# Optimization experiments

Hardware: AMD Instinct MI355X
Metric: run time of the kernel (lower is better)

## Reference

```python
import jax, jax.numpy as jnp
import numpy as np

HEADS = 16
D_K = 64  # hidden_units // heads


def setup_inputs() -> dict:
    key = jax.random.key(0)
    ks = jax.random.split(key, 9)
    B, S, D, H = 4, 2048, 1024, 1024  # batch, seq, in_shape, hidden_units
    inputs = jax.random.normal(ks[0], (B, S, D), dtype=jnp.float32)
    # xavier_normal for weights, default bias init ~ small uniform (use zeros for simplicity of baseline? keep uniform like torch)
    def xavier(k, fan_in, fan_out):
        std = jnp.sqrt(2.0 / (fan_in + fan_out))
        return jax.random.normal(k, (fan_out, fan_in), dtype=jnp.float32) * std
    Wq = xavier(ks[1], D, H)
    Wk = xavier(ks[2], D, H)
    Wv = xavier(ks[3], D, H)
    Wo = xavier(ks[4], H, H)
    bound = 1.0 / jnp.sqrt(D)
    bq = jax.random.uniform(ks[5], (H,), minval=-bound, maxval=bound, dtype=jnp.float32)
    bk = jax.random.uniform(ks[6], (H,), minval=-bound, maxval=bound, dtype=jnp.float32)
    bv = jax.random.uniform(ks[7], (H,), minval=-bound, maxval=bound, dtype=jnp.float32)
    bo = jax.random.uniform(ks[8], (H,), minval=-1.0 / jnp.sqrt(H), maxval=1.0 / jnp.sqrt(H), dtype=jnp.float32)
    return {"inputs": inputs, "Wq": Wq, "bq": bq, "Wk": Wk, "bk": bk,
            "Wv": Wv, "bv": bv, "Wo": Wo, "bo": bo}


def reference(inputs, Wq, bq, Wk, bk, Wv, bv, Wo, bo):
    B, S, _ = inputs.shape
    # QKV projections -> (B, S, heads, d_k)
    def proj(W, b):
        return (inputs @ W.T + b).reshape(B, S, HEADS, D_K)
    q = proj(Wq, bq)
    k = proj(Wk, bk)
    v = proj(Wv, bv)
    scale = 1.0 / jnp.sqrt(jnp.float32(D_K))
    # scores: (B, heads, S, S)
    scores = jnp.einsum('bqhd,bkhd->bhqk', q, k) * scale
    attn = jax.nn.softmax(scores, axis=-1)
    # (B, heads, S, d_k) -> (B, S, heads*d_k)
    ctx = jnp.einsum('bhqk,bkhd->bqhd', attn, v).reshape(B, S, HEADS * D_K)
    out = ctx @ Wo.T + bo
    return out
```

## Files before the change

kernel.cpp:

```cpp
#include <hip/hip_runtime.h>
#include <stdint.h>


using bf16x8 = __attribute__((ext_vector_type(8))) short;
using f32x4  = __attribute__((ext_vector_type(4))) float;

#define QSCALE 0.18033688f

__device__ __forceinline__ unsigned short f2bf(float f) {
    unsigned u = __builtin_bit_cast(unsigned, f);
    u += 0x7fffu + ((u >> 16) & 1u);
    return (unsigned short)(u >> 16);
}

__device__ __forceinline__ unsigned pack2bf(float f0, float f1) {
    unsigned u0 = __builtin_bit_cast(unsigned, f0) + 0x8000u;
    unsigned u1 = __builtin_bit_cast(unsigned, f1) + 0x8000u;
    return __builtin_amdgcn_perm(u1, u0, 0x07060302);
}

__device__ __forceinline__ void gld16(const void* g, void* l) {
    void* gnc = (void*)g;
    __builtin_amdgcn_global_load_lds((__attribute__((address_space(1))) void*)gnc,
                                     (__attribute__((address_space(3))) void*)l,
                                     16, 0, 0);
}

__device__ __forceinline__ int swz(int R, int g) {
    return R * 64 + ((g ^ (R & 7)) << 3);
}

__global__ void castall(const float* __restrict__ X, const float* __restrict__ Wq,
                        const float* __restrict__ Wk, const float* __restrict__ Wv,
                        const float* __restrict__ Wo, unsigned short* __restrict__ Xb,
                        unsigned short* __restrict__ Wqkvb, unsigned short* __restrict__ Wob) {
    const int bx = blockIdx.x;
    const float* src; unsigned short* dst; int idx;
    if (bx < 8192) { src = X; dst = Xb; idx = bx * 256 + threadIdx.x; }
    else {
        const int r = bx - 8192, w = r >> 10;
        idx = (r & 1023) * 256 + threadIdx.x;
        src = (w == 0) ? Wq : (w == 1) ? Wk : (w == 2) ? Wv : Wo;
        dst = (w == 3) ? Wob : Wqkvb + (size_t)w * 1048576;
    }
    float4 v = ((const float4*)src)[idx];
    ((uint2*)dst)[idx] = make_uint2(pack2bf(v.x, v.y), pack2bf(v.z, v.w));
}

__global__ __launch_bounds__(256) void gemm_qkv(const unsigned short* __restrict__ A,
                                                const unsigned short* __restrict__ Wqkv,
                                                const float* __restrict__ bq,
                                                const float* __restrict__ bk,
                                                const float* __restrict__ bv,
                                                unsigned short* __restrict__ Qb,
                                                unsigned short* __restrict__ Kb,
                                                unsigned short* __restrict__ Vt) {
    __shared__ alignas(16) unsigned short smem[17408];
    unsigned short* sA = smem;
    unsigned short* sB = smem + 8192;
    unsigned short* OT = smem;

    const int tid  = threadIdx.x;
    const int lane = tid & 63;
    const int wave = tid >> 6;
    const int quad = lane >> 4;
    const int l15  = lane & 15;
    const int lr   = lane >> 3;
    const int lcs  = (((lane & 7) ^ lr) << 3);
    const int nb   = blockIdx.x >> 3;
    const int col0 = (blockIdx.x & 7) * 128;
    const int row0 = blockIdx.y * 128;
    const unsigned short* W = Wqkv + ((size_t)nb << 20);
    const float* bias = (nb == 0) ? bq : (nb == 1) ? bk : bv;
    const int wm = wave >> 1, wn = wave & 1;

    f32x4 acc[4][4];
#pragma unroll
    for (int i = 0; i < 4; i++)
#pragma unroll
        for (int j = 0; j < 4; j++) acc[i][j] = f32x4{0.f, 0.f, 0.f, 0.f};

    for (int kt = 0; kt < 16; ++kt) {
        const int k0 = kt * 64;
#pragma unroll
        for (int i = 0; i < 4; i++) {
            const int c = wave * 4 + i;
            const int r = c * 8 + lr;
            gld16(A + (size_t)(row0 + r) * 1024 + k0 + lcs, &sA[c * 512]);
            gld16(W + (size_t)(col0 + r) * 1024 + k0 + lcs, &sB[c * 512]);
        }
        __syncthreads();
#pragma unroll
        for (int kx = 0; kx < 2; ++kx) {
            bf16x8 a[4], b[4];
#pragma unroll
            for (int i = 0; i < 4; i++) {
                a[i] = *(const bf16x8*)&sA[swz(wm * 64 + i * 16 + l15, kx * 4 + quad)];
                b[i] = *(const bf16x8*)&sB[swz(wn * 64 + i * 16 + l15, kx * 4 + quad)];
            }
#pragma unroll
            for (int i = 0; i < 4; i++)
#pragma unroll
                for (int j = 0; j < 4; j++)
                    acc[i][j] = __builtin_amdgcn_mfma_f32_16x16x32_bf16(a[i], b[j], acc[i][j], 0, 0, 0);
        }
        __syncthreads();
    }

    if (nb != 2) {
        const float sc = (nb == 0) ? QSCALE : 1.0f;
#pragma unroll
        for (int i = 0; i < 4; i++) {
#pragma unroll
            for (int j = 0; j < 4; j++) {
                const int ct  = wn * 64 + j * 16 + l15;
                const float bvv = bias[col0 + ct];
                const int rt  = wm * 64 + i * 16 + quad * 4;
#pragma unroll
                for (int r = 0; r < 4; r++)
                    OT[(rt + r) * 136 + ct] = f2bf((acc[i][j][r] + bvv) * sc);
            }
        }
    } else {
#pragma unroll
        for (int i = 0; i < 4; i++) {
#pragma unroll
            for (int j = 0; j < 4; j++) {
                const int ct  = wn * 64 + j * 16 + l15;
                const float bvv = bias[col0 + ct];
                const int rt  = wm * 64 + i * 16 + quad * 4;
                *(uint2*)&OT[ct * 136 + rt] =
                    make_uint2(pack2bf(acc[i][j][0] + bvv, acc[i][j][1] + bvv),
                               pack2bf(acc[i][j][2] + bvv, acc[i][j][3] + bvv));
            }
        }
    }
    __syncthreads();

    const int rr   = wave * 32 + (lane >> 1);
    const int half = lane & 1;
    if (nb != 2) {
        unsigned short* C = (nb == 0) ? Qb : Kb;
        unsigned short* gdst = C + (size_t)(row0 + rr) * 1024 + col0 + half * 64;
#pragma unroll
        for (int k = 0; k < 8; k++)
            *(bf16x8*)(gdst + k * 8) = *(const bf16x8*)&OT[rr * 136 + half * 64 + k * 8];
    } else {
        const int bb = row0 >> 11, s0l = row0 & 2047;
        unsigned short* gdst = Vt + ((size_t)(bb * 1024 + col0 + rr)) * 2048 + s0l + half * 64;
#pragma unroll
        for (int k = 0; k < 8; k++)
            *(bf16x8*)(gdst + k * 8) = *(const bf16x8*)&OT[rr * 136 + half * 64 + k * 8];
    }
}

__global__ __launch_bounds__(256) void gemm_out(const unsigned short* __restrict__ A,
                                                const unsigned short* __restrict__ W,
                                                const float* __restrict__ bias,
                                                float* __restrict__ C) {
    __shared__ alignas(16) unsigned short sA[128 * 64];
    __shared__ alignas(16) unsigned short sB[128 * 64];
    const int tid  = threadIdx.x;
    const int lane = tid & 63;
    const int wave = tid >> 6;
    const int quad = lane >> 4;
    const int l15  = lane & 15;
    const int lr   = lane >> 3;
    const int lcs  = (((lane & 7) ^ lr) << 3);
    const int row0 = blockIdx.y * 128;
    const int col0 = blockIdx.x * 128;
    const int wm = wave >> 1, wn = wave & 1;

    f32x4 acc[4][4];
#pragma unroll
    for (int i = 0; i < 4; i++)
#pragma unroll
        for (int j = 0; j < 4; j++) acc[i][j] = f32x4{0.f, 0.f, 0.f, 0.f};

    for (int kt = 0; kt < 16; ++kt) {
        const int k0 = kt * 64;
#pragma unroll
        for (int i = 0; i < 4; i++) {
            const int c = wave * 4 + i;
            const int r = c * 8 + lr;
            gld16(A + (size_t)(row0 + r) * 1024 + k0 + lcs, &sA[c * 512]);
            gld16(W + (size_t)(col0 + r) * 1024 + k0 + lcs, &sB[c * 512]);
        }
        __syncthreads();
#pragma unroll
        for (int kx = 0; kx < 2; ++kx) {
            bf16x8 a[4], b[4];
#pragma unroll
            for (int i = 0; i < 4; i++) {
                a[i] = *(const bf16x8*)&sA[swz(wm * 64 + i * 16 + l15, kx * 4 + quad)];
                b[i] = *(const bf16x8*)&sB[swz(wn * 64 + i * 16 + l15, kx * 4 + quad)];
            }
#pragma unroll
            for (int i = 0; i < 4; i++)
#pragma unroll
                for (int j = 0; j < 4; j++)
                    acc[i][j] = __builtin_amdgcn_mfma_f32_16x16x32_bf16(a[i], b[j], acc[i][j], 0, 0, 0);
        }
        __syncthreads();
    }

#pragma unroll
    for (int i = 0; i < 4; i++) {
#pragma unroll
        for (int j = 0; j < 4; j++) {
            const int col   = col0 + wn * 64 + j * 16 + l15;
            const float bvv = bias[col];
            const int rbase = row0 + wm * 64 + i * 16 + quad * 4;
#pragma unroll
            for (int r = 0; r < 4; r++)
                C[(size_t)(rbase + r) * 1024 + col] = acc[i][j][r] + bvv;
        }
    }
}

__global__ __launch_bounds__(512) void attn(const unsigned short* __restrict__ Q,
                                            const unsigned short* __restrict__ K,
                                            const unsigned short* __restrict__ Vt,
                                            unsigned short* __restrict__ Ctx) {
    __shared__ alignas(16) unsigned short Kl[2][4096];
    __shared__ alignas(16) unsigned short Vl[2][4096];
    __shared__ alignas(16) unsigned short Pl[8][32][72];

    const int tid  = threadIdx.x;
    const int lane = tid & 63;
    const int wave = tid >> 6;
    const int quad = lane >> 4;
    const int l15  = lane & 15;
    const int lr   = lane >> 3;
    const int lcs  = (((lane & 7) ^ lr) << 3);

    const int qt = blockIdx.x, h = blockIdx.y, b = blockIdx.z;
    const int q0 = qt * 256;
    const size_t tokbase = (size_t)b * 2048;

    bf16x8 qa[2][2];
#pragma unroll
    for (int mt = 0; mt < 2; ++mt)
#pragma unroll
        for (int kx = 0; kx < 2; ++kx)
            qa[mt][kx] = *(const bf16x8*)(Q + (tokbase + q0 + wave * 32 + mt * 16 + l15) * 1024 +
                                          h * 64 + kx * 32 + quad * 8);

    f32x4 O[2][4], Osum[2];
#pragma unroll
    for (int mt = 0; mt < 2; ++mt) {
#pragma unroll
        for (int nt = 0; nt < 4; ++nt) O[mt][nt] = f32x4{0.f, 0.f, 0.f, 0.f};
        Osum[mt] = f32x4{0.f, 0.f, 0.f, 0.f};
    }
    const bf16x8 vones = {16256, 16256, 16256, 16256, 16256, 16256, 16256, 16256};

#define AT_STAGE(kt_, buf_)                                                                     \
    {                                                                                           \
        const int rr = wave * 8 + lr;                                                           \
        gld16(K + (tokbase + (kt_) * 64 + rr) * 1024 + h * 64 + lcs, &Kl[buf_][wave * 512]);    \
        gld16(Vt + ((size_t)(b * 1024 + h * 64 + rr)) * 2048 + (kt_) * 64 + lcs,                \
              &Vl[buf_][wave * 512]);                                                           \
    }

    AT_STAGE(0, 0)
    for (int kt = 0; kt < 32; ++kt) {
        const int buf = kt & 1;
        __syncthreads();
        if (kt < 31) AT_STAGE(kt + 1, buf ^ 1)

        f32x4 St[4][2];
#pragma unroll
        for (int nt = 0; nt < 4; ++nt)
#pragma unroll
            for (int mt = 0; mt < 2; ++mt) St[nt][mt] = f32x4{0.f, 0.f, 0.f, 0.f};
#pragma unroll
        for (int kx = 0; kx < 2; ++kx) {
            bf16x8 kb[4];
#pragma unroll
            for (int nt = 0; nt < 4; ++nt)
                kb[nt] = *(const bf16x8*)&Kl[buf][swz(nt * 16 + l15, kx * 4 + quad)];
#pragma unroll
            for (int nt = 0; nt < 4; ++nt)
#pragma unroll
                for (int mt = 0; mt < 2; ++mt)
                    St[nt][mt] = __builtin_amdgcn_mfma_f32_16x16x32_bf16(kb[nt], qa[mt][kx], St[nt][mt], 0, 0, 0);
        }

#pragma unroll
        for (int mt = 0; mt < 2; ++mt) {
#pragma unroll
            for (int nt = 0; nt < 4; ++nt) {
                float p0 = __builtin_amdgcn_exp2f(St[nt][mt][0]);
                float p1 = __builtin_amdgcn_exp2f(St[nt][mt][1]);
                float p2 = __builtin_amdgcn_exp2f(St[nt][mt][2]);
                float p3 = __builtin_amdgcn_exp2f(St[nt][mt][3]);
                *(uint2*)&Pl[wave][mt * 16 + l15][nt * 16 + quad * 4] =
                    make_uint2(pack2bf(p0, p1), pack2bf(p2, p3));
            }
        }

#pragma unroll
        for (int kx = 0; kx < 2; ++kx) {
            bf16x8 pa[2], vb[4];
#pragma unroll
            for (int mt = 0; mt < 2; ++mt)
                pa[mt] = *(const bf16x8*)&Pl[wave][mt * 16 + l15][kx * 32 + quad * 8];
#pragma unroll
            for (int nt = 0; nt < 4; ++nt)
                vb[nt] = *(const bf16x8*)&Vl[buf][swz(nt * 16 + l15, kx * 4 + quad)];
#pragma unroll
            for (int mt = 0; mt < 2; ++mt) {
#pragma unroll
                for (int nt = 0; nt < 4; ++nt)
                    O[mt][nt] = __builtin_amdgcn_mfma_f32_16x16x32_bf16(pa[mt], vb[nt], O[mt][nt], 0, 0, 0);
                Osum[mt] = __builtin_amdgcn_mfma_f32_16x16x32_bf16(pa[mt], vones, Osum[mt], 0, 0, 0);
            }
        }
    }
#undef AT_STAGE

#pragma unroll
    for (int mt = 0; mt < 2; ++mt) {
#pragma unroll
        for (int r = 0; r < 4; ++r) {
            const float inv = 1.0f / Osum[mt][r];
            const int row   = q0 + wave * 32 + mt * 16 + quad * 4 + r;
            const size_t base = (tokbase + row) * 1024 + h * 64;
#pragma unroll
            for (int nt = 0; nt < 4; ++nt)
                Ctx[base + nt * 16 + l15] = f2bf(O[mt][nt][r] * inv);
        }
    }
}

extern "C" void kernel_launch(void* const* d_in, const int* in_sizes, int n_in,
                              void* d_out, int out_size, void* d_ws, size_t ws_size,
                              hipStream_t stream) {
    (void)in_sizes; (void)n_in; (void)out_size; (void)ws_size;
    const float* X  = (const float*)d_in[0];
    const float* Wq = (const float*)d_in[1];
    const float* bq = (const float*)d_in[2];
    const float* Wk = (const float*)d_in[3];
    const float* bk = (const float*)d_in[4];
    const float* Wv = (const float*)d_in[5];
    const float* bv = (const float*)d_in[6];
    const float* Wo = (const float*)d_in[7];
    const float* bo = (const float*)d_in[8];

    char* ws = (char*)d_ws;
    unsigned short* Xb    = (unsigned short*)(ws);
    unsigned short* Qb    = (unsigned short*)(ws + (size_t)16 * 1048576);
    unsigned short* Kb    = (unsigned short*)(ws + (size_t)32 * 1048576);
    unsigned short* Vt    = (unsigned short*)(ws + (size_t)48 * 1048576);
    unsigned short* Wqkvb = (unsigned short*)(ws + (size_t)64 * 1048576);
    unsigned short* Wob   = (unsigned short*)(ws + (size_t)70 * 1048576);
    unsigned short* Ctx   = Xb;

    castall<<<dim3(12288), 256, 0, stream>>>(X, Wq, Wk, Wv, Wo, Xb, Wqkvb, Wob);
    gemm_qkv<<<dim3(24, 64), 256, 0, stream>>>(Xb, Wqkvb, bq, bk, bv, Qb, Kb, Vt);
    attn<<<dim3(8, 16, 4), 512, 0, stream>>>(Qb, Kb, Vt, Ctx);
    gemm_out<<<dim3(8, 64), 256, 0, stream>>>(Ctx, Wob, bo, (float*)d_out);
}
```

Baseline: 277.1 us.

## Rewrite QKV GEMM with 256x256 tiles and double-buffered async LDS pipeline

The QKV projection GEMM moves from 128x128 tiles with 4 waves and a synchronous load-then-compute loop to 256x256 tiles with 8 waves, using 128KB of LDS as two buffers. Global-to-LDS loads for the next k-tile are interleaved with MFMA phases, paced by explicit vmcnt waits and barriers, and MFMA bursts run at raised wave priority. This targets memory latency stalls and raises data reuse per tile. The trade-off is fewer blocks (384), more registers and LDS per block, and an epilogue split into two halves.

Measured after the change: 293.1 us. 5.8% more time.

```diff
diff --git a/kernel.cpp b/kernel.cpp
--- a/kernel.cpp
+++ b/kernel.cpp
@@ -47,110 +47,159 @@
     ((uint2*)dst)[idx] = make_uint2(pack2bf(v.x, v.y), pack2bf(v.z, v.w));
 }
 
-__global__ __launch_bounds__(256) void gemm_qkv(const unsigned short* __restrict__ A,
-                                                const unsigned short* __restrict__ Wqkv,
-                                                const float* __restrict__ bq,
-                                                const float* __restrict__ bk,
-                                                const float* __restrict__ bv,
-                                                unsigned short* __restrict__ Qb,
-                                                unsigned short* __restrict__ Kb,
-                                                unsigned short* __restrict__ Vt) {
-    __shared__ alignas(16) unsigned short smem[17408];
-    unsigned short* sA = smem;
-    unsigned short* sB = smem + 8192;
-    unsigned short* OT = smem;
+__global__ __launch_bounds__(512, 2) void gemm_qkv(const unsigned short* __restrict__ A,
+                                                   const unsigned short* __restrict__ Wqkv,
+                                                   const float* __restrict__ bq,
+                                                   const float* __restrict__ bk,
+                                                   const float* __restrict__ bv,
+                                                   unsigned short* __restrict__ Qb,
+                                                   unsigned short* __restrict__ Kb,
+                                                   unsigned short* __restrict__ Vt) {
+    __shared__ alignas(16) unsigned short smem[65536];
 
     const int tid  = threadIdx.x;
     const int lane = tid & 63;
-    const int wave = tid >> 6;
+    const int w    = tid >> 6;
     const int quad = lane >> 4;
     const int l15  = lane & 15;
     const int lr   = lane >> 3;
     const int lcs  = (((lane & 7) ^ lr) << 3);
-    const int nb   = blockIdx.x >> 3;
-    const int col0 = (blockIdx.x & 7) * 128;
-    const int row0 = blockIdx.y * 128;
-    const unsigned short* W = Wqkv + ((size_t)nb << 20);
+    const int wm   = w >> 2;
+    const int wn   = w & 3;
+
+    const int col0 = blockIdx.x * 256;
+    const int row0 = blockIdx.y * 256;
+
+    const unsigned short* aS = A    + (size_t)(row0 + w * 16 + lr) * 1024 + lcs;
+    const unsigned short* bS = Wqkv + (size_t)(col0 + w * 16 + lr) * 1024 + lcs;
+    const int dstW = w * 1024;
+
+#define STG_A(t_, h_, b_)                                                              \
+    { const unsigned short* s_ = aS + (size_t)(h_) * 131072 + (t_) * 64;               \
+      gld16(s_,            &smem[(b_) * 32768 + (h_) * 8192 + dstW]);                  \
+      gld16(s_ + 8 * 1024, &smem[(b_) * 32768 + (h_) * 8192 + dstW + 512]); }
+#define STG_B(t_, h_, b_)                                                              \
+    { const unsigned short* s_ = bS + (size_t)(h_) * 131072 + (t_) * 64;               \
+      gld16(s_,            &smem[(b_) * 32768 + 16384 + (h_) * 8192 + dstW]);          \
+      gld16(s_ + 8 * 1024, &smem[(b_) * 32768 + 16384 + (h_) * 8192 + dstW + 512]); }
+
+    f32x4 acc[8][4];
+#pragma unroll
+    for (int i = 0; i < 8; i++)
+#pragma unroll
+        for (int j = 0; j < 4; j++) acc[i][j] = f32x4{0.f, 0.f, 0.f, 0.f};
+
+    STG_A(0, 0, 0) STG_A(0, 1, 0) STG_B(0, 0, 0) STG_B(0, 1, 0)
+    STG_B(1, 0, 1) STG_B(1, 1, 1)
+    asm volatile("s_waitcnt vmcnt(4)" ::: "memory");
+    __builtin_amdgcn_s_barrier();
+
+    for (int t = 0; t < 16; ++t) {
+        const int b = t & 1;
+        unsigned short* bufA = smem + b * 32768;
+        unsigned short* bufB = bufA + 16384;
+        bf16x8 bfr[4][2];
+#pragma unroll
+        for (int p = 0; p < 4; ++p) {
+            bf16x8 afr[2][2];
+            if (p == 0) {
+#pragma unroll
+                for (int nf = 0; nf < 4; ++nf)
+#pragma unroll
+                    for (int kx = 0; kx < 2; ++kx)
+                        bfr[nf][kx] = *(const bf16x8*)&bufB[swz(wn * 64 + nf * 16 + l15, kx * 4 + quad)];
+            }
+#pragma unroll
+            for (int mi = 0; mi < 2; ++mi)
+#pragma unroll
+                for (int kx = 0; kx < 2; ++kx)
+                    afr[mi][kx] = *(const bf16x8*)&bufA[swz(wm * 128 + (p * 2 + mi) * 16 + l15, kx * 4 + quad)];
+
+            if (p == 0)      { if (t < 15) STG_A(t + 1, 0, b ^ 1) }
+            else if (p == 1) { if (t < 15) STG_A(t + 1, 1, b ^ 1) }
+            else if (p == 2) { if (t < 14) STG_B(t + 2, 0, b) }
+            else {
+                if (t < 14) {
+                    STG_B(t + 2, 1, b)
+                    asm volatile("s_waitcnt vmcnt(4)" ::: "memory");
+                } else if (t == 14) {
+                    asm volatile("s_waitcnt vmcnt(0)" ::: "memory");
+                }
+            }
+            __builtin_amdgcn_s_barrier();
+            asm volatile("s_waitcnt lgkmcnt(0)" ::: "memory");
+            __builtin_amdgcn_sched_barrier(0);
+            __builtin_amdgcn_s_setprio(1);
+#pragma unroll
+            for (int kx = 0; kx < 2; ++kx)
+#pragma unroll
+                for (int mi = 0; mi < 2; ++mi)
+#pragma unroll
+                    for (int nf = 0; nf < 4; ++nf)
+                        acc[p * 2 + mi][nf] = __builtin_amdgcn_mfma_f32_16x16x32_bf16(
+                            afr[mi][kx], bfr[nf][kx], acc[p * 2 + mi][nf], 0, 0, 0);
+            __builtin_amdgcn_s_setprio(0);
+            __builtin_amdgcn_s_barrier();
+        }
+    }
+#undef STG_A
+#undef STG_B
+
+    const int nb   = col0 >> 10;
+    const int colq = col0 & 1023;
     const float* bias = (nb == 0) ? bq : (nb == 1) ? bk : bv;
-    const int wm = wave >> 1, wn = wave & 1;
-
-    f32x4 acc[4][4];
-#pragma unroll
-    for (int i = 0; i < 4; i++)
-#pragma unroll
-        for (int j = 0; j < 4; j++) acc[i][j] = f32x4{0.f, 0.f, 0.f, 0.f};
-
-    for (int kt = 0; kt < 16; ++kt) {
-        const int k0 = kt * 64;
-#pragma unroll
-        for (int i = 0; i < 4; i++) {
-            const int c = wave * 4 + i;
-            const int r = c * 8 + lr;
-            gld16(A + (size_t)(row0 + r) * 1024 + k0 + lcs, &sA[c * 512]);
-            gld16(W + (size_t)(col0 + r) * 1024 + k0 + lcs, &sB[c * 512]);
-        }
-        __syncthreads();
-#pragma unroll
-        for (int kx = 0; kx < 2; ++kx) {
-            bf16x8 a[4], b[4];
-#pragma unroll
-            for (int i = 0; i < 4; i++) {
-                a[i] = *(const bf16x8*)&sA[swz(wm * 64 + i * 16 + l15, kx * 4 + quad)];
-                b[i] = *(const bf16x8*)&sB[swz(wn * 64 + i * 16 + l15, kx * 4 + quad)];
-            }
-#pragma unroll
-            for (int i = 0; i < 4; i++)
-#pragma unroll
-                for (int j = 0; j < 4; j++)
-                    acc[i][j] = __builtin_amdgcn_mfma_f32_16x16x32_bf16(a[i], b[j], acc[i][j], 0, 0, 0);
-        }
-        __syncthreads();
-    }
 
     if (nb != 2) {
         const float sc = (nb == 0) ? QSCALE : 1.0f;
-#pragma unroll
-        for (int i = 0; i < 4; i++) {
-#pragma unroll
-            for (int j = 0; j < 4; j++) {
-                const int ct  = wn * 64 + j * 16 + l15;
-                const float bvv = bias[col0 + ct];
-                const int rt  = wm * 64 + i * 16 + quad * 4;
-#pragma unroll
-                for (int r = 0; r < 4; r++)
-                    OT[(rt + r) * 136 + ct] = f2bf((acc[i][j][r] + bvv) * sc);
-            }
+        unsigned short* C = (nb == 0) ? Qb : Kb;
+#pragma unroll
+        for (int h = 0; h < 2; ++h) {
+            if (wm == h) {
+#pragma unroll
+                for (int mf = 0; mf < 8; ++mf)
+#pragma unroll
+                    for (int nf = 0; nf < 4; ++nf) {
+                        const int ct  = wn * 64 + nf * 16 + l15;
+                        const float bvv = bias[colq + ct];
+                        const int rt  = mf * 16 + quad * 4;
+#pragma unroll
+                        for (int r = 0; r < 4; ++r)
+                            smem[(rt + r) * 264 + ct] = f2bf((acc[mf][nf][r] + bvv) * sc);
+                    }
+            }
+            __syncthreads();
+            const int rr = tid >> 2, qq = tid & 3;
+            unsigned short* gdst = C + (size_t)(row0 + h * 128 + rr) * 1024 + colq + qq * 64;
+#pragma unroll
+            for (int j = 0; j < 8; ++j)
+                *(bf16x8*)(gdst + j * 8) = *(const bf16x8*)&smem[rr * 264 + qq * 64 + j * 8];
+            if (h == 0) __syncthreads();
         }
     } else {
-#pragma unroll
-        for (int i = 0; i < 4; i++) {
-#pragma unroll
-            for (int j = 0; j < 4; j++) {
-                const int ct  = wn * 64 + j * 16 + l15;
-                const float bvv = bias[col0 + ct];
-                const int rt  = wm * 64 + i * 16 + quad * 4;
-                *(uint2*)&OT[ct * 136 + rt] =
-                    make_uint2(pack2bf(acc[i][j][0] + bvv, acc[i][j][1] + bvv),
-                               pack2bf(acc[i][j][2] + bvv, acc[i][j][3] + bvv));
-            }
-        }
-    }
-    __syncthreads();
-
-    const int rr   = wave * 32 + (lane >> 1);
-    const int half = lane & 1;
-    if (nb != 2) {
-        unsigned short* C = (nb == 0) ? Qb : Kb;
-        unsigned short* gdst = C + (size_t)(row0 + rr) * 1024 + col0 + half * 64;
-#pragma unroll
-        for (int k = 0; k < 8; k++)
-            *(bf16x8*)(gdst + k * 8) = *(const bf16x8*)&OT[rr * 136 + half * 64 + k * 8];
-    } else {
-        const int bb = row0 >> 11, s0l = row0 & 2047;
-        unsigned short* gdst = Vt + ((size_t)(bb * 1024 + col0 + rr)) * 2048 + s0l + half * 64;
-#pragma unroll
-        for (int k = 0; k < 8; k++)
-            *(bf16x8*)(gdst + k * 8) = *(const bf16x8*)&OT[rr * 136 + half * 64 + k * 8];
+        const int bb = row0 >> 11, s0 = row0 & 2047;
+#pragma unroll
+        for (int h = 0; h < 2; ++h) {
+            if (wm == h) {
+#pragma unroll
+                for (int mf = 0; mf < 8; ++mf)
+#pragma unroll
+                    for (int nf = 0; nf < 4; ++nf) {
+                        const int ct  = wn * 64 + nf * 16 + l15;
+                        const float bvv = bias[colq + ct];
+                        const int st  = mf * 16 + quad * 4;
+                        *(uint2*)&smem[ct * 136 + st] =
+                            make_uint2(pack2bf(acc[mf][nf][0] + bvv, acc[mf][nf][1] + bvv),
+                                       pack2bf(acc[mf][nf][2] + bvv, acc[mf][nf][3] + bvv));
+                    }
+            }
+            __syncthreads();
+            const int c = tid >> 1, hs = tid & 1;
+            unsigned short* gdst = Vt + ((size_t)(bb * 1024 + colq + c)) * 2048 + s0 + h * 128 + hs * 64;
+#pragma unroll
+            for (int j = 0; j < 8; ++j)
+                *(bf16x8*)(gdst + j * 8) = *(const bf16x8*)&smem[c * 136 + hs * 64 + j * 8];
+            if (h == 0) __syncthreads();
+        }
     }
 }
 
@@ -358,7 +407,7 @@
     unsigned short* Ctx   = Xb;
 
     castall<<<dim3(12288), 256, 0, stream>>>(X, Wq, Wk, Wv, Wo, Xb, Wqkvb, Wob);
-    gemm_qkv<<<dim3(24, 64), 256, 0, stream>>>(Xb, Wqkvb, bq, bk, bv, Qb, Kb, Vt);
+    gemm_qkv<<<dim3(12, 32), 512, 0, stream>>>(Xb, Wqkvb, bq, bk, bv, Qb, Kb, Vt);
     attn<<<dim3(8, 16, 4), 512, 0, stream>>>(Qb, Kb, Vt, Ctx);
     gemm_out<<<dim3(8, 64), 256, 0, stream>>>(Ctx, Wob, bo, (float*)d_out);
 }
```
